# Kernel optimization log

Measured on AMD Instinct MI355X. Metric: run time of the kernel, lower is better.

Reference implementation:

```python
import jax, jax.numpy as jnp
import numpy as np
import math

H = 32          # num_heads
D = 128         # head_dim
HID = 2048      # hidden_size
INNER = H * D   # hidden_inner_size
BLOCK = 256
NUM_LAYERS = 32
LAYER_IDX = 0


def build_slopes(n):
    def p2(m):
        start = 2 ** (-(2 ** (-(math.log2(m) - 3))))
        return [start * (start ** i) for i in range(m)]
    if math.log2(n).is_integer():
        s = p2(n)
    else:
        c = 2 ** math.floor(math.log2(n))
        s = p2(c) + p2(2 * c)[0::2][: n - c]
    s = np.asarray(s, dtype=np.float32)
    s = s * (1.0 - LAYER_IDX / (NUM_LAYERS - 1) + 1e-5)
    return jnp.asarray(s)  # [H]


def lightning_attention(q, k, v, slope, kv0, block):
    # q,k,v: [h,n,d]; slope: [h]; kv0: [h,d,e]
    h, n, d = q.shape
    nb = n // block
    arr = jnp.arange(1, block + 1, dtype=jnp.float32)            # [m]
    s = slope[:, None, None]                                      # [h,1,1]
    q_decay = jnp.exp(-s * arr[None, :, None])                    # [h,m,1]
    k_decay = jnp.exp(-s * (block - arr)[None, :, None])          # [h,m,1]
    idx = arr[:, None] - arr[None, :]                             # [m,m]
    diag_decay = jnp.where(idx >= 0, jnp.exp(-s * idx), 0.0)      # [h,m,m]
    blk_decay = jnp.exp(-slope * block)[:, None, None]            # [h,1,1]

    qb = q.reshape(h, nb, block, d).transpose(1, 0, 2, 3)         # [nb,h,m,d]
    kb = k.reshape(h, nb, block, d).transpose(1, 0, 2, 3)
    vb = v.reshape(h, nb, block, d).transpose(1, 0, 2, 3)

    def step(kv, blk):
        qi, ki, vi = blk
        inter = jnp.einsum('hmd,hde->hme', qi * q_decay, kv)
        qk = jnp.einsum('hmd,hnd->hmn', qi, ki) * diag_decay
        intra = jnp.einsum('hmn,hne->hme', qk, vi)
        kv_new = blk_decay * kv + jnp.einsum('hmd,hme->hde', ki * k_decay, vi)
        return kv_new, inter + intra

    kv_final, out = jax.lax.scan(step, kv0, (qb, kb, vb))
    out = out.transpose(1, 0, 2, 3).reshape(h, n, d)
    return out, kv_final


def rmsnorm(x, w, eps=1e-5):
    xf = x.astype(jnp.float32)
    var = jnp.mean(xf * xf, axis=-1, keepdims=True)
    return (xf * jax.lax.rsqrt(var + eps)).astype(x.dtype) * w


def setup_inputs() -> dict:
    key = jax.random.key(0)
    ks = jax.random.split(key, 4)
    n = 4096
    return {
        'hidden_states': jax.random.normal(ks[0], (n, HID), dtype=jnp.float32),
        'positions': jnp.arange(n, dtype=jnp.int64) if jax.config.jax_enable_x64 else jnp.arange(n, dtype=jnp.int32),
        'kv_cache': jnp.zeros((H, D, D), dtype=jnp.float32),
        'W_qkv': jax.random.normal(ks[1], (HID, 3 * INNER), dtype=jnp.float32) / np.sqrt(HID),
        'W_gate': jax.random.normal(ks[2], (HID, INNER), dtype=jnp.float32) / np.sqrt(HID),
        'W_out': jax.random.normal(ks[3], (INNER, HID), dtype=jnp.float32) / np.sqrt(INNER),
        'norm_weight': jnp.ones((INNER,), dtype=jnp.float32),
    }


def reference(hidden_states, positions, kv_cache, W_qkv, W_gate, W_out, norm_weight):
    n = hidden_states.shape[0]
    slope = build_slopes(H)
    qkv = hidden_states @ W_qkv                                # [n, 3*INNER]
    act = jax.nn.silu(qkv.astype(jnp.float32)).reshape(n, H, 3 * D)
    q, k, v = jnp.split(act, 3, axis=-1)                       # [n,H,D] each
    q = q.transpose(1, 0, 2)                                   # [H,n,D]
    k = k.transpose(1, 0, 2)
    v = v.transpose(1, 0, 2)
    attn, kv_final = lightning_attention(q, k, v, slope, kv_cache.astype(jnp.float32), BLOCK)
    hidden = attn.transpose(1, 0, 2).reshape(n, INNER)          # n (h d)
    hidden = rmsnorm(hidden, norm_weight)
    gate = hidden_states @ W_gate
    hidden = jax.nn.sigmoid(gate) * hidden
    out = hidden @ W_out                                        # [n, HID]
    return out
```

## Files before the change

### kernel.cpp

```cpp
#include <hip/hip_runtime.h>
#include <hip/hip_bf16.h>
#include <cstdint>
#include <cstddef>

#define SEQ    4096
#define HEADS  32
#define HD     128
#define HIDDEN 2048
#define NINNER 4096
#define BLK    256
#define NB     16

typedef __attribute__((ext_vector_type(8)))  __bf16 bf16x8;
typedef __attribute__((ext_vector_type(4)))  __bf16 bf16x4;
typedef __attribute__((ext_vector_type(4)))  float  f32x4;

#define MFMA16(a,b,c) __builtin_amdgcn_mfma_f32_16x16x32_bf16((a),(b),(c),0,0,0)

typedef __attribute__((address_space(1))) const unsigned int gu32;
typedef __attribute__((address_space(3))) unsigned int lu32;

__device__ __forceinline__ void gld16(void* lds, const void* g){
    __builtin_amdgcn_global_load_lds((gu32*)g, (lu32*)lds, 16, 0, 0);
}

__device__ __forceinline__ float slope_for_head(int h){
    return exp2f(-0.25f*(float)(h+1)) * 1.00001f;
}

__device__ __forceinline__ void tcast_block(const float* __restrict__ W, __bf16* __restrict__ Wt,
                                            int K, int N, int bx, int by, __bf16 (*t)[72], int tid){
    const int n0 = bx*64, k0 = by*64;
    const int r = tid >> 4, c4 = tid & 15;
    #pragma unroll
    for (int i = 0; i < 4; i++){
        int k = r + i*16;
        float4 v = *(const float4*)(W + (size_t)(k0 + k)*N + n0 + c4*4);
        t[c4*4+0][k] = (__bf16)v.x;
        t[c4*4+1][k] = (__bf16)v.y;
        t[c4*4+2][k] = (__bf16)v.z;
        t[c4*4+3][k] = (__bf16)v.w;
    }
    __syncthreads();
    #pragma unroll
    for (int j = 0; j < 2; j++){
        int idx = tid + j*256;
        int n = idx >> 3, c8 = idx & 7;
        bf16x8 val = *(const bf16x8*)&t[n][c8*8];
        *(bf16x8*)(Wt + (size_t)(n0 + n)*K + k0 + c8*8) = val;
    }
}

__global__ __launch_bounds__(256)
void prep_all(const float* __restrict__ hs, __bf16* __restrict__ hsb,
              const float* __restrict__ Wqkv, __bf16* __restrict__ WqkvT,
              const float* __restrict__ Wgate, __bf16* __restrict__ WgateT,
              const float* __restrict__ Wout, __bf16* __restrict__ WoutT)
{
    __shared__ __align__(16) __bf16 t[64][72];
    const int tid = threadIdx.x;
    int id = blockIdx.x;
    if (id < 8192){
        int i = (id*256 + tid)*4;
        float4 v = *(const float4*)(hs + i);
        bf16x4 o;
        o[0] = (__bf16)v.x; o[1] = (__bf16)v.y; o[2] = (__bf16)v.z; o[3] = (__bf16)v.w;
        *(bf16x4*)(hsb + i) = o;
    } else if (id < 14336){
        int j = id - 8192;
        tcast_block(Wqkv, WqkvT, 2048, 12288, j % 192, j / 192, t, tid);
    } else if (id < 16384){
        int j = id - 14336;
        tcast_block(Wgate, WgateT, 2048, 4096, j % 64, j / 64, t, tid);
    } else {
        int j = id - 16384;
        tcast_block(Wout, WoutT, 4096, 2048, j % 32, j / 32, t, tid);
    }
}

template<int EPI>
__global__ __launch_bounds__(256,2)
void gemm_bt(const __bf16* __restrict__ A, const __bf16* __restrict__ Bt,
             float* __restrict__ Cf,
             __bf16* __restrict__ qbuf, __bf16* __restrict__ kbuf,
             __bf16* __restrict__ kT,   __bf16* __restrict__ vT,
             __bf16* __restrict__ sgate,
             int M, int N, int K)
{
    __shared__ __align__(16) __bf16 a_lds[128*64];
    __shared__ __align__(16) __bf16 b_lds[128*64];
    const int tid  = threadIdx.x;
    const int lane = tid & 63;
    const int w    = tid >> 6;
    const int lr   = lane & 15;
    const int quad = lane >> 4;
    const int wm = w & 1, wn = w >> 1;

    int bm, bn;
    if constexpr (EPI == 0){
        int id = blockIdx.x;
        bm = id & 31;
        bn = (id >> 9)*16 + ((id >> 5) & 15);
    } else {
        bm = blockIdx.x & 31;
        bn = blockIdx.x >> 5;
    }

    f32x4 acc[4][4];
    #pragma unroll
    for (int i = 0; i < 4; i++)
        #pragma unroll
        for (int j = 0; j < 4; j++) acc[i][j] = (f32x4){0.f,0.f,0.f,0.f};

    const int r8 = lane >> 3;
    const int qs = (lane & 7) ^ r8;
    const int sw = lr & 7;
    const __bf16* Abase = A  + (size_t)bm*128*K;
    const __bf16* Bbase = Bt + (size_t)bn*128*K;

    for (int kb = 0; kb < K; kb += 64){
        #pragma unroll
        for (int t = 0; t < 4; t++){
            int ch = t*4 + w;
            gld16(a_lds + ch*512, Abase + (size_t)(ch*8 + r8)*K + kb + qs*8);
            gld16(b_lds + ch*512, Bbase + (size_t)(ch*8 + r8)*K + kb + qs*8);
        }
        __syncthreads();
        #pragma unroll
        for (int kk = 0; kk < 2; kk++){
            bf16x8 af[4];
            #pragma unroll
            for (int mt = 0; mt < 4; mt++)
                af[mt] = *(const bf16x8*)&a_lds[(wm*64 + mt*16 + lr)*64 + (((kk*4+quad) ^ sw)*8)];
            #pragma unroll
            for (int nt = 0; nt < 4; nt++){
                bf16x8 bfv = *(const bf16x8*)&b_lds[(wn*64 + nt*16 + lr)*64 + (((kk*4+quad) ^ sw)*8)];
                #pragma unroll
                for (int mt = 0; mt < 4; mt++)
                    acc[mt][nt] = MFMA16(af[mt], bfv, acc[mt][nt]);
            }
        }
        __syncthreads();
    }

    if constexpr (EPI == 0){
        if (bn < 96){
            const int h = bn / 3, which = bn % 3;
            const float s = slope_for_head(h);
            if (which == 0){
                #pragma unroll
                for (int mt = 0; mt < 4; mt++)
                #pragma unroll
                for (int nt = 0; nt < 4; nt++)
                #pragma unroll
                for (int r = 0; r < 4; r++){
                    int pos = bm*128 + wm*64 + mt*16 + quad*4 + r;
                    int d = wn*64 + nt*16 + lr;
                    float x = acc[mt][nt][r];
                    float sv = x / (1.f + __expf(-x));
                    qbuf[((size_t)h*SEQ + pos)*HD + d] = (__bf16)sv;
                }
            } else if (which == 1){
                const float es1 = __expf(s);
                #pragma unroll
                for (int mt = 0; mt < 4; mt++)
                #pragma unroll
                for (int nt = 0; nt < 4; nt++){
                    const int d = wn*64 + nt*16 + lr;
                    const int pos0 = bm*128 + wm*64 + mt*16 + quad*4;
                    float dec = __expf(-s*(float)(255 - (pos0 & 255)));
                    bf16x4 pk;
                    #pragma unroll
                    for (int r = 0; r < 4; r++){
                        float x = acc[mt][nt][r];
                        float sv = x / (1.f + __expf(-x));
                        kbuf[((size_t)h*SEQ + pos0 + r)*HD + d] = (__bf16)sv;
                        pk[r] = (__bf16)(sv*dec);
                        dec *= es1;
                    }
                    *(bf16x4*)(kT + ((size_t)h*HD + d)*SEQ + pos0) = pk;
                }
            } else {
                #pragma unroll
                for (int mt = 0; mt < 4; mt++)
                #pragma unroll
                for (int nt = 0; nt < 4; nt++){
                    const int d = wn*64 + nt*16 + lr;
                    const int pos0 = bm*128 + wm*64 + mt*16 + quad*4;
                    bf16x4 pv;
                    #pragma unroll
                    for (int r = 0; r < 4; r++){
                        float x = acc[mt][nt][r];
                        pv[r] = (__bf16)(x / (1.f + __expf(-x)));
                    }
                    *(bf16x4*)(vT + ((size_t)h*HD + d)*SEQ + pos0) = pv;
                }
            }
        } else {
            const int col0 = (bn - 96)*128;
            #pragma unroll
            for (int mt = 0; mt < 4; mt++)
            #pragma unroll
            for (int nt = 0; nt < 4; nt++)
            #pragma unroll
            for (int r = 0; r < 4; r++){
                int row = bm*128 + wm*64 + mt*16 + quad*4 + r;
                int col = col0 + wn*64 + nt*16 + lr;
                float x = acc[mt][nt][r];
                sgate[(size_t)row*NINNER + col] = (__bf16)(1.f/(1.f + __expf(-x)));
            }
        }
    } else {
        #pragma unroll
        for (int mt = 0; mt < 4; mt++)
        #pragma unroll
        for (int nt = 0; nt < 4; nt++)
        #pragma unroll
        for (int r = 0; r < 4; r++){
            int row = bm*128 + wm*64 + mt*16 + quad*4 + r;
            int col = bn*128 + wn*64 + nt*16 + lr;
            Cf[(size_t)row*N + col] = acc[mt][nt][r];
        }
    }
}

__global__ __launch_bounds__(256,2)
void pass_a(const __bf16* __restrict__ vT, const __bf16* __restrict__ kT,
            float* __restrict__ kvbT)
{
    __shared__ __align__(16) __bf16 a_lds[128*64];
    __shared__ __align__(16) __bf16 b_lds[128*64];
    const int b = blockIdx.x, h = blockIdx.y;
    const int tid = threadIdx.x, lane = tid & 63, w = tid >> 6;
    const int lr = lane & 15, quad = lane >> 4;
    const int wm = w & 1, wn = w >> 1;

    f32x4 acc[4][4];
    #pragma unroll
    for (int i = 0; i < 4; i++)
        #pragma unroll
        for (int j = 0; j < 4; j++) acc[i][j] = (f32x4){0.f,0.f,0.f,0.f};

    const int r8 = lane >> 3;
    const int qs = (lane & 7) ^ r8;
    const int sw = lr & 7;
    const __bf16* Abase = vT + (size_t)h*HD*SEQ + (size_t)b*BLK;
    const __bf16* Bbase = kT + (size_t)h*HD*SEQ + (size_t)b*BLK;

    for (int kb = 0; kb < BLK; kb += 64){
        #pragma unroll
        for (int t = 0; t < 4; t++){
            int ch = t*4 + w;
            gld16(a_lds + ch*512, Abase + (size_t)(ch*8 + r8)*SEQ + kb + qs*8);
            gld16(b_lds + ch*512, Bbase + (size_t)(ch*8 + r8)*SEQ + kb + qs*8);
        }
        __syncthreads();
        #pragma unroll
        for (int kk = 0; kk < 2; kk++){
            bf16x8 af[4];
            #pragma unroll
            for (int mt = 0; mt < 4; mt++)
                af[mt] = *(const bf16x8*)&a_lds[(wm*64 + mt*16 + lr)*64 + (((kk*4+quad) ^ sw)*8)];
            #pragma unroll
            for (int nt = 0; nt < 4; nt++){
                bf16x8 bfv = *(const bf16x8*)&b_lds[(wn*64 + nt*16 + lr)*64 + (((kk*4+quad) ^ sw)*8)];
                #pragma unroll
                for (int mt = 0; mt < 4; mt++)
                    acc[mt][nt] = MFMA16(af[mt], bfv, acc[mt][nt]);
            }
        }
        __syncthreads();
    }
    float* outp = kvbT + (size_t)(h*NB + b)*HD*HD;
    #pragma unroll
    for (int mt = 0; mt < 4; mt++)
    #pragma unroll
    for (int nt = 0; nt < 4; nt++)
    #pragma unroll
    for (int r = 0; r < 4; r++){
        int row = wm*64 + mt*16 + quad*4 + r;
        int col = wn*64 + nt*16 + lr;
        outp[(size_t)row*HD + col] = acc[mt][nt][r];
    }
}

__global__ __launch_bounds__(256)
void scan_kv(const float* __restrict__ kvbT, const float* __restrict__ kv0,
             __bf16* __restrict__ kvsT)
{
    const int chunk = blockIdx.x;
    const int h = blockIdx.y;
    const int t = threadIdx.x;
    const float s = slope_for_head(h);
    const float lam = __expf(-s*(float)BLK);
    const int le0 = chunk*2048;
    float st[8], cur[8], nxt[8];
    #pragma unroll
    for (int j = 0; j < 8; j++){
        int le = le0 + t + 256*j;
        int e = le >> 7, d = le & 127;
        st[j] = kv0[(size_t)h*HD*HD + (size_t)d*HD + e];
    }
    size_t base0 = (size_t)(h*NB)*HD*HD + le0;
    #pragma unroll
    for (int j = 0; j < 8; j++) cur[j] = kvbT[base0 + t + 256*j];
    for (int b = 0; b < NB; b++){
        size_t base = (size_t)(h*NB + b)*HD*HD + le0;
        #pragma unroll
        for (int j = 0; j < 8; j++) kvsT[base + t + 256*j] = (__bf16)st[j];
        if (b < NB-1){
            size_t nb = base + (size_t)HD*HD;
            #pragma unroll
            for (int j = 0; j < 8; j++) nxt[j] = kvbT[nb + t + 256*j];
        }
        #pragma unroll
        for (int j = 0; j < 8; j++){ st[j] = lam*st[j] + cur[j]; cur[j] = nxt[j]; }
    }
}

__global__ __launch_bounds__(256,2)
void pass_c(const __bf16* __restrict__ qbuf, const __bf16* __restrict__ kbuf,
            const __bf16* __restrict__ vT, const __bf16* __restrict__ kvsT,
            float* __restrict__ attn)
{
    __shared__ __align__(16) __bf16 p_lds[4][32*72];
    const int rb = blockIdx.x & 1, b = blockIdx.x >> 1, h = blockIdx.y;
    const float s = slope_for_head(h);
    const int tid = threadIdx.x, lane = tid & 63, w = tid >> 6;
    const int lr = lane & 15, quad = lane >> 4;
    const int R0 = rb*128 + w*32;

    const __bf16* qh  = qbuf + (size_t)h*SEQ*HD + (size_t)b*BLK*HD;
    const __bf16* kh  = kbuf + (size_t)h*SEQ*HD + (size_t)b*BLK*HD;
    const __bf16* vh  = vT   + (size_t)h*HD*SEQ + (size_t)b*BLK;
    const __bf16* kvh = kvsT + (size_t)(h*NB + b)*HD*HD;

    f32x4 acc[2][8];
    #pragma unroll
    for (int i = 0; i < 2; i++)
        #pragma unroll
        for (int j = 0; j < 8; j++) acc[i][j] = (f32x4){0.f,0.f,0.f,0.f};

    bf16x8 qf[4][2];
    #pragma unroll
    for (int ks = 0; ks < 4; ks++)
        #pragma unroll
        for (int mt = 0; mt < 2; mt++)
            qf[ks][mt] = *(const bf16x8*)(qh + (size_t)(R0 + mt*16 + lr)*HD + ks*32 + quad*8);

    float qdec[2];
    #pragma unroll
    for (int mt = 0; mt < 2; mt++)
        qdec[mt] = __expf(-s*(float)(R0 + mt*16 + lr + 1));
    #pragma unroll
    for (int ks = 0; ks < 4; ks++){
        bf16x8 saf[2];
        #pragma unroll
        for (int mt = 0; mt < 2; mt++)
            #pragma unroll
            for (int j = 0; j < 8; j++) saf[mt][j] = (__bf16)((float)qf[ks][mt][j]*qdec[mt]);
        #pragma unroll
        for (int nt = 0; nt < 8; nt++){
            bf16x8 bv = *(const bf16x8*)(kvh + (size_t)(nt*16 + lr)*HD + ks*32 + quad*8);
            #pragma unroll
            for (int mt = 0; mt < 2; mt++) acc[mt][nt] = MFMA16(saf[mt], bv, acc[mt][nt]);
        }
    }

    float colf[4];
    #pragma unroll
    for (int nt = 0; nt < 4; nt++)
        colf[nt] = __expf(-s*(float)(63 - nt*16 - lr));
    const int cmax = (R0 + 31) >> 6;
    for (int c = 0; c <= cmax; c++){
        f32x4 qk[2][4];
        #pragma unroll
        for (int i = 0; i < 2; i++)
            #pragma unroll
            for (int j = 0; j < 4; j++) qk[i][j] = (f32x4){0.f,0.f,0.f,0.f};
        #pragma unroll
        for (int ks = 0; ks < 4; ks++){
            #pragma unroll
            for (int nt = 0; nt < 4; nt++){
                bf16x8 kf = *(const bf16x8*)(kh + (size_t)(c*64 + nt*16 + lr)*HD + ks*32 + quad*8);
                #pragma unroll
                for (int mt = 0; mt < 2; mt++) qk[mt][nt] = MFMA16(qf[ks][mt], kf, qk[mt][nt]);
            }
        }
        float rowf[2][4];
        #pragma unroll
        for (int mt = 0; mt < 2; mt++)
            #pragma unroll
            for (int r = 0; r < 4; r++)
                rowf[mt][r] = __expf(-s*(float)(R0 + mt*16 + quad*4 + r - c*64 - 63));
        #pragma unroll
        for (int mt = 0; mt < 2; mt++)
        #pragma unroll
        for (int nt = 0; nt < 4; nt++)
        #pragma unroll
        for (int r = 0; r < 4; r++){
            int i  = R0 + mt*16 + quad*4 + r;
            int jj = c*64 + nt*16 + lr;
            float dv = (i >= jj) ? rowf[mt][r]*colf[nt] : 0.f;
            p_lds[w][(mt*16 + quad*4 + r)*72 + nt*16 + lr] = (__bf16)(qk[mt][nt][r]*dv);
        }
        #pragma unroll
        for (int ks2 = 0; ks2 < 2; ks2++){
            bf16x8 pf[2];
            #pragma unroll
            for (int mt = 0; mt < 2; mt++)
                pf[mt] = *(const bf16x8*)&p_lds[w][(mt*16 + lr)*72 + ks2*32 + quad*8];
            #pragma unroll
            for (int nt = 0; nt < 8; nt++){
                bf16x8 vf = *(const bf16x8*)(vh + (size_t)(nt*16 + lr)*SEQ + c*64 + ks2*32 + quad*8);
                #pragma unroll
                for (int mt = 0; mt < 2; mt++) acc[mt][nt] = MFMA16(pf[mt], vf, acc[mt][nt]);
            }
        }
    }

    #pragma unroll
    for (int mt = 0; mt < 2; mt++)
    #pragma unroll
    for (int nt = 0; nt < 8; nt++)
    #pragma unroll
    for (int r = 0; r < 4; r++){
        int pos = b*BLK + R0 + mt*16 + quad*4 + r;
        int e = nt*16 + lr;
        attn[(size_t)pos*NINNER + h*HD + e] = acc[mt][nt][r];
    }
}

__global__ __launch_bounds__(256)
void rmsgate(const float* __restrict__ attn, const __bf16* __restrict__ sg,
             const float* __restrict__ nw, __bf16* __restrict__ h2)
{
    const int row = blockIdx.x, tid = threadIdx.x;
    const float* x = attn + (size_t)row*NINNER;
    float4 xs[4];
    float ss = 0.f;
    #pragma unroll
    for (int i = 0; i < 4; i++){
        xs[i] = *(const float4*)(x + (i*256 + tid)*4);
        ss += xs[i].x*xs[i].x + xs[i].y*xs[i].y + xs[i].z*xs[i].z + xs[i].w*xs[i].w;
    }
    #pragma unroll
    for (int o = 32; o > 0; o >>= 1) ss += __shfl_down(ss, o, 64);
    __shared__ float red[4];
    const int lane = tid & 63, w = tid >> 6;
    if (lane == 0) red[w] = ss;
    __syncthreads();
    float tot = red[0] + red[1] + red[2] + red[3];
    float rs = rsqrtf(tot*(1.f/NINNER) + 1e-5f);
    #pragma unroll
    for (int i = 0; i < 4; i++){
        int idx = (i*256 + tid)*4;
        float4 wv = *(const float4*)(nw + idx);
        bf16x4 sv = *(const bf16x4*)(sg + (size_t)row*NINNER + idx);
        bf16x4 o;
        o[0] = (__bf16)((float)sv[0] * xs[i].x*rs*wv.x);
        o[1] = (__bf16)((float)sv[1] * xs[i].y*rs*wv.y);
        o[2] = (__bf16)((float)sv[2] * xs[i].z*rs*wv.z);
        o[3] = (__bf16)((float)sv[3] * xs[i].w*rs*wv.w);
        *(bf16x4*)(h2 + (size_t)row*NINNER + idx) = o;
    }
}

extern "C" void kernel_launch(void* const* d_in, const int* in_sizes, int n_in,
                              void* d_out, int out_size, void* d_ws, size_t ws_size,
                              hipStream_t stream) {
    (void)in_sizes; (void)n_in; (void)out_size; (void)ws_size;
    const float* hs    = (const float*)d_in[0];
    const float* kv0   = (const float*)d_in[2];
    const float* Wqkv  = (const float*)d_in[3];
    const float* Wgate = (const float*)d_in[4];
    const float* Wout  = (const float*)d_in[5];
    const float* nw    = (const float*)d_in[6];
    float* out = (float*)d_out;

    char* ws = (char*)d_ws;
    __bf16* WqkvT  = (__bf16*)(ws);
    __bf16* WgateT = (__bf16*)(ws + 50331648);
    float*  attn   = (float*)(ws);
    __bf16* WoutT  = (__bf16*)(ws + 67108864);
    __bf16* hsb    = (__bf16*)(ws + 83886080);
    __bf16* qkvb   = (__bf16*)(ws + 100663296);
    __bf16* qbuf   = qkvb;
    __bf16* kbuf   = qkvb + (size_t)HEADS*SEQ*HD;
    __bf16* h2     = qkvb;
    __bf16* kT     = (__bf16*)(ws + 201326592);
    __bf16* vT     = (__bf16*)(ws + 234881024);
    float*  kvbT   = (float*) (ws + 268435456);
    __bf16* kvsT   = (__bf16*)(ws + 301989888);
    __bf16* sgate  = (__bf16*)(ws + 318767104);

    prep_all<<<18432, 256, 0, stream>>>(hs, hsb, Wqkv, WqkvT, Wgate, WgateT, Wout, WoutT);

    gemm_bt<0><<<4096, 256, 0, stream>>>(hsb, WqkvT, nullptr, qbuf, kbuf, kT, vT, sgate,
                                         4096, 16384, 2048);

    pass_a<<<dim3(16, 32), 256, 0, stream>>>(vT, kT, kvbT);
    scan_kv<<<dim3(8, 32), 256, 0, stream>>>(kvbT, kv0, kvsT);
    pass_c<<<dim3(NB*2, 32), 256, 0, stream>>>(qbuf, kbuf, vT, kvsT, attn);

    rmsgate<<<4096, 256, 0, stream>>>(attn, sgate, nw, h2);
    gemm_bt<2><<<512, 256, 0, stream>>>(h2, WoutT, out, nullptr, nullptr, nullptr, nullptr, nullptr,
                                        4096, 2048, 4096);
}
```

Baseline: 740.7 us.

## Add dedicated 256x256 double-buffered QKV+gate GEMM with ping-pong MFMA scheduling

Replaces the generic 128x128 gemm_bt for the fused QKV/gate projection with a new 512-thread kernel that computes 256x256 tiles. The K loop is double-buffered in LDS and uses direct global-to-LDS loads, interleaved with MFMA phases separated by barriers and s_setprio, plus an XCD-aware block remap. The aim is higher arithmetic intensity and overlap of global loads with matrix math in the largest GEMM. The cost is more LDS and registers per block (8x4 accumulators), which lowers occupancy, and a hand-tuned waitcnt schedule that must stay correct.

```diff
diff --git a/kernel.cpp b/kernel.cpp
--- a/kernel.cpp
+++ b/kernel.cpp
@@ -82,9 +82,6 @@
 __global__ __launch_bounds__(256,2)
 void gemm_bt(const __bf16* __restrict__ A, const __bf16* __restrict__ Bt,
              float* __restrict__ Cf,
-             __bf16* __restrict__ qbuf, __bf16* __restrict__ kbuf,
-             __bf16* __restrict__ kT,   __bf16* __restrict__ vT,
-             __bf16* __restrict__ sgate,
              int M, int N, int K)
 {
     __shared__ __align__(16) __bf16 a_lds[128*64];
@@ -96,15 +93,8 @@
     const int quad = lane >> 4;
     const int wm = w & 1, wn = w >> 1;
 
-    int bm, bn;
-    if constexpr (EPI == 0){
-        int id = blockIdx.x;
-        bm = id & 31;
-        bn = (id >> 9)*16 + ((id >> 5) & 15);
-    } else {
-        bm = blockIdx.x & 31;
-        bn = blockIdx.x >> 5;
-    }
+    const int bm = blockIdx.x & 31;
+    const int bn = blockIdx.x >> 5;
 
     f32x4 acc[4][4];
     #pragma unroll
@@ -143,32 +133,175 @@
         __syncthreads();
     }
 
-    if constexpr (EPI == 0){
-        if (bn < 96){
-            const int h = bn / 3, which = bn % 3;
-            const float s = slope_for_head(h);
-            if (which == 0){
-                #pragma unroll
-                for (int mt = 0; mt < 4; mt++)
-                #pragma unroll
-                for (int nt = 0; nt < 4; nt++)
-                #pragma unroll
-                for (int r = 0; r < 4; r++){
-                    int pos = bm*128 + wm*64 + mt*16 + quad*4 + r;
-                    int d = wn*64 + nt*16 + lr;
-                    float x = acc[mt][nt][r];
-                    float sv = x / (1.f + __expf(-x));
-                    qbuf[((size_t)h*SEQ + pos)*HD + d] = (__bf16)sv;
+    #pragma unroll
+    for (int mt = 0; mt < 4; mt++)
+    #pragma unroll
+    for (int nt = 0; nt < 4; nt++)
+    #pragma unroll
+    for (int r = 0; r < 4; r++){
+        int row = bm*128 + wm*64 + mt*16 + quad*4 + r;
+        int col = bn*128 + wn*64 + nt*16 + lr;
+        Cf[(size_t)row*N + col] = acc[mt][nt][r];
+    }
+}
+
+__global__ __launch_bounds__(512, 2)
+void gemm_qkv(const __bf16* __restrict__ A, const __bf16* __restrict__ Bt,
+              __bf16* __restrict__ qbuf, __bf16* __restrict__ kbuf,
+              __bf16* __restrict__ kT,   __bf16* __restrict__ vT,
+              __bf16* __restrict__ sgate)
+{
+    __shared__ __align__(16) __bf16 lds[2][2][2][8192];
+
+    const int tid  = threadIdx.x;
+    const int lane = tid & 63;
+    const int w    = tid >> 6;
+    const int wm   = w & 1;
+    const int wn   = w >> 1;
+    const int lr   = lane & 15;
+    const int quad = lane >> 4;
+
+    const int id  = blockIdx.x;
+    const int wg  = (id & 7)*128 + (id >> 3);
+    const int bm  = wg & 15;
+    const int bn2 = wg >> 4;
+
+    const int l3   = lane >> 3;
+    const int lgs  = (lane & 7) ^ l3;
+    const int srow = l3*2 + (lgs >> 2);
+    const int sg   = lgs & 3;
+
+    const int ag   = ((((lane & 1) << 2) | quad) ^ ((lr >> 1) & 7)) * 8;
+    const int aoff = (wm*64 + (lr >> 1))*64 + ag;
+    const int boff = (wn*32 + (lr >> 1))*64 + ag;
+
+    const __bf16* Abase = A  + (size_t)bm*256*2048;
+    const __bf16* Bbase = Bt + (size_t)bn2*256*2048;
+
+    auto stage = [&](int ab, int buf, int kh, const __bf16* Base, int tcol){
+        #pragma unroll
+        for (int j = 0; j < 2; j++){
+            const int ch = j*8 + w;
+            gld16(&lds[ab][buf][kh][ch*512],
+                  Base + (size_t)(ch*16 + srow)*2048 + tcol + kh*32 + sg*8);
+        }
+    };
+
+    f32x4 acc[8][4];
+    #pragma unroll
+    for (int i = 0; i < 8; i++)
+        #pragma unroll
+        for (int j = 0; j < 4; j++) acc[i][j] = (f32x4){0.f,0.f,0.f,0.f};
+
+    bf16x8 af[8], bf0, bf1;
+
+    stage(0, 0, 0, Abase, 0);
+    stage(1, 0, 0, Bbase, 0);
+    stage(0, 0, 1, Abase, 0);
+    stage(1, 0, 1, Bbase, 0);
+    asm volatile("s_waitcnt vmcnt(4)" ::: "memory");
+    __builtin_amdgcn_s_barrier();
+
+    for (int t = 0; t < 32; t++){
+        const int c = t & 1, nbuf = c ^ 1;
+        const bool pf = (t + 1 < 32);
+        const int tcol = (t + 1)*64;
+
+        #pragma unroll
+        for (int mt = 0; mt < 8; mt++)
+            af[mt] = *(const bf16x8*)&lds[0][c][0][aoff + mt*512];
+        bf0 = *(const bf16x8*)&lds[1][c][0][boff];
+        bf1 = *(const bf16x8*)&lds[1][c][0][boff + 512];
+        if (pf) stage(0, nbuf, 0, Abase, tcol);
+        __builtin_amdgcn_s_barrier();
+        asm volatile("s_waitcnt lgkmcnt(0)" ::: "memory");
+        __builtin_amdgcn_s_setprio(1);
+        #pragma unroll
+        for (int mt = 0; mt < 8; mt++){
+            acc[mt][0] = MFMA16(af[mt], bf0, acc[mt][0]);
+            acc[mt][1] = MFMA16(af[mt], bf1, acc[mt][1]);
+        }
+        __builtin_amdgcn_s_setprio(0);
+        __builtin_amdgcn_s_barrier();
+
+        bf0 = *(const bf16x8*)&lds[1][c][0][boff + 1024];
+        bf1 = *(const bf16x8*)&lds[1][c][0][boff + 1536];
+        if (pf) stage(1, nbuf, 0, Bbase, tcol);
+        __builtin_amdgcn_s_barrier();
+        asm volatile("s_waitcnt lgkmcnt(0)" ::: "memory");
+        __builtin_amdgcn_s_setprio(1);
+        #pragma unroll
+        for (int mt = 0; mt < 8; mt++){
+            acc[mt][2] = MFMA16(af[mt], bf0, acc[mt][2]);
+            acc[mt][3] = MFMA16(af[mt], bf1, acc[mt][3]);
+        }
+        __builtin_amdgcn_s_setprio(0);
+        if (pf) { asm volatile("s_waitcnt vmcnt(4)" ::: "memory"); }
+        else    { asm volatile("s_waitcnt vmcnt(0)" ::: "memory"); }
+        __builtin_amdgcn_s_barrier();
+
+        #pragma unroll
+        for (int mt = 0; mt < 8; mt++)
+            af[mt] = *(const bf16x8*)&lds[0][c][1][aoff + mt*512];
+        bf0 = *(const bf16x8*)&lds[1][c][1][boff];
+        bf1 = *(const bf16x8*)&lds[1][c][1][boff + 512];
+        if (pf) stage(0, nbuf, 1, Abase, tcol);
+        __builtin_amdgcn_s_barrier();
+        asm volatile("s_waitcnt lgkmcnt(0)" ::: "memory");
+        __builtin_amdgcn_s_setprio(1);
+        #pragma unroll
+        for (int mt = 0; mt < 8; mt++){
+            acc[mt][0] = MFMA16(af[mt], bf0, acc[mt][0]);
+            acc[mt][1] = MFMA16(af[mt], bf1, acc[mt][1]);
+        }
+        __builtin_amdgcn_s_setprio(0);
+        __builtin_amdgcn_s_barrier();
+
+        bf0 = *(const bf16x8*)&lds[1][c][1][boff + 1024];
+        bf1 = *(const bf16x8*)&lds[1][c][1][boff + 1536];
+        if (pf) stage(1, nbuf, 1, Bbase, tcol);
+        __builtin_amdgcn_s_barrier();
+        asm volatile("s_waitcnt lgkmcnt(0)" ::: "memory");
+        __builtin_amdgcn_s_setprio(1);
+        #pragma unroll
+        for (int mt = 0; mt < 8; mt++){
+            acc[mt][2] = MFMA16(af[mt], bf0, acc[mt][2]);
+            acc[mt][3] = MFMA16(af[mt], bf1, acc[mt][3]);
+        }
+        __builtin_amdgcn_s_setprio(0);
+        asm volatile("s_waitcnt vmcnt(4)" ::: "memory");
+        __builtin_amdgcn_s_barrier();
+    }
+
+    const int bn_old = bn2*2 + (wn >> 1);
+    const int dbase  = (wn & 1)*64;
+    if (bn_old < 96){
+        const int h = bn_old/3, which = bn_old - h*3;
+        const float s = slope_for_head(h);
+        if (which == 0){
+            #pragma unroll
+            for (int mt = 0; mt < 8; mt++){
+                const int pos0 = bm*256 + wm*128 + mt*16 + quad*4;
+                #pragma unroll
+                for (int nt = 0; nt < 4; nt++){
+                    const int d = dbase + nt*16 + lr;
+                    #pragma unroll
+                    for (int r = 0; r < 4; r++){
+                        float x = acc[mt][nt][r];
+                        qbuf[((size_t)h*SEQ + pos0 + r)*HD + d] = (__bf16)(x / (1.f + __expf(-x)));
+                    }
                 }
-            } else if (which == 1){
-                const float es1 = __expf(s);
-                #pragma unroll
-                for (int mt = 0; mt < 4; mt++)
+            }
+        } else if (which == 1){
+            const float es1 = __expf(s);
+            #pragma unroll
+            for (int mt = 0; mt < 8; mt++){
+                const int pos0 = bm*256 + wm*128 + mt*16 + quad*4;
+                const float dec0 = __expf(-s*(float)(255 - (pos0 & 255)));
                 #pragma unroll
                 for (int nt = 0; nt < 4; nt++){
-                    const int d = wn*64 + nt*16 + lr;
-                    const int pos0 = bm*128 + wm*64 + mt*16 + quad*4;
-                    float dec = __expf(-s*(float)(255 - (pos0 & 255)));
+                    const int d = dbase + nt*16 + lr;
+                    float dec = dec0;
                     bf16x4 pk;
                     #pragma unroll
                     for (int r = 0; r < 4; r++){
@@ -180,13 +313,14 @@
                     }
                     *(bf16x4*)(kT + ((size_t)h*HD + d)*SEQ + pos0) = pk;
                 }
-            } else {
-                #pragma unroll
-                for (int mt = 0; mt < 4; mt++)
+            }
+        } else {
+            #pragma unroll
+            for (int mt = 0; mt < 8; mt++){
+                const int pos0 = bm*256 + wm*128 + mt*16 + quad*4;
                 #pragma unroll
                 for (int nt = 0; nt < 4; nt++){
-                    const int d = wn*64 + nt*16 + lr;
-                    const int pos0 = bm*128 + wm*64 + mt*16 + quad*4;
+                    const int d = dbase + nt*16 + lr;
                     bf16x4 pv;
                     #pragma unroll
                     for (int r = 0; r < 4; r++){
@@ -196,30 +330,21 @@
                     *(bf16x4*)(vT + ((size_t)h*HD + d)*SEQ + pos0) = pv;
                 }
             }
-        } else {
-            const int col0 = (bn - 96)*128;
-            #pragma unroll
-            for (int mt = 0; mt < 4; mt++)
-            #pragma unroll
-            for (int nt = 0; nt < 4; nt++)
-            #pragma unroll
-            for (int r = 0; r < 4; r++){
-                int row = bm*128 + wm*64 + mt*16 + quad*4 + r;
-                int col = col0 + wn*64 + nt*16 + lr;
-                float x = acc[mt][nt][r];
-                sgate[(size_t)row*NINNER + col] = (__bf16)(1.f/(1.f + __expf(-x)));
-            }
         }
     } else {
-        #pragma unroll
-        for (int mt = 0; mt < 4; mt++)
-        #pragma unroll
-        for (int nt = 0; nt < 4; nt++)
-        #pragma unroll
-        for (int r = 0; r < 4; r++){
-            int row = bm*128 + wm*64 + mt*16 + quad*4 + r;
-            int col = bn*128 + wn*64 + nt*16 + lr;
-            Cf[(size_t)row*N + col] = acc[mt][nt][r];
+        const int col0 = (bn_old - 96)*128 + dbase;
+        #pragma unroll
+        for (int mt = 0; mt < 8; mt++){
+            const int pos0 = bm*256 + wm*128 + mt*16 + quad*4;
+            #pragma unroll
+            for (int nt = 0; nt < 4; nt++){
+                const int col = col0 + nt*16 + lr;
+                #pragma unroll
+                for (int r = 0; r < 4; r++){
+                    float x = acc[mt][nt][r];
+                    sgate[(size_t)(pos0 + r)*NINNER + col] = (__bf16)(1.f/(1.f + __expf(-x)));
+                }
+            }
         }
     }
 }
@@ -496,14 +621,12 @@
 
     prep_all<<<18432, 256, 0, stream>>>(hs, hsb, Wqkv, WqkvT, Wgate, WgateT, Wout, WoutT);
 
-    gemm_bt<0><<<4096, 256, 0, stream>>>(hsb, WqkvT, nullptr, qbuf, kbuf, kT, vT, sgate,
-                                         4096, 16384, 2048);
+    gemm_qkv<<<1024, 512, 0, stream>>>(hsb, WqkvT, qbuf, kbuf, kT, vT, sgate);
 
     pass_a<<<dim3(16, 32), 256, 0, stream>>>(vT, kT, kvbT);
     scan_kv<<<dim3(8, 32), 256, 0, stream>>>(kvbT, kv0, kvsT);
     pass_c<<<dim3(NB*2, 32), 256, 0, stream>>>(qbuf, kbuf, vT, kvsT, attn);
 
     rmsgate<<<4096, 256, 0, stream>>>(attn, sgate, nw, h2);
-    gemm_bt<2><<<512, 256, 0, stream>>>(h2, WoutT, out, nullptr, nullptr, nullptr, nullptr, nullptr,
-                                        4096, 2048, 4096);
-}
+    gemm_bt<2><<<512, 256, 0, stream>>>(h2, WoutT, out, 4096, 2048, 4096);
+}
```

Result: faster. 715.1 us (-3.5%).
